# Kernel tuning notes

Hardware: AMD Instinct MI355X
Metric: run time of the kernel (lower is better)

Reference implementation:

```python
import jax, jax.numpy as jnp
import numpy as np

B, T, D, H = 64, 512, 512, 512

def setup_inputs() -> dict:
    key = jax.random.key(0)
    ks = jax.random.split(key, 9)
    std = 0.01
    return {
        "X": jax.random.normal(ks[0], (B, T, D), jnp.float32),
        "W_xi": std * jax.random.normal(ks[1], (D, H), jnp.float32),
        "W_hi": std * jax.random.normal(ks[2], (H, H), jnp.float32),
        "b_i": jnp.zeros((H,), jnp.float32),
        "W_xf": std * jax.random.normal(ks[3], (D, H), jnp.float32),
        "W_hf": std * jax.random.normal(ks[4], (H, H), jnp.float32),
        "b_f": jnp.zeros((H,), jnp.float32),
        "W_xo": std * jax.random.normal(ks[5], (D, H), jnp.float32),
        "W_ho": std * jax.random.normal(ks[6], (H, H), jnp.float32),
        "b_o": jnp.zeros((H,), jnp.float32),
        "W_xc": std * jax.random.normal(ks[7], (D, H), jnp.float32),
        "W_hc": std * jax.random.normal(ks[8], (H, H), jnp.float32),
        "b_c": jnp.zeros((H,), jnp.float32),
    }


def _lstm(X, W_xi, W_hi, b_i, W_xf, W_hf, b_f, W_xo, W_ho, b_o, W_xc, W_hc, b_c):
    # Fuse the 4 gate weight matrices into single GEMMs (same math as 8
    # separate matmuls in the original).
    W_x = jnp.concatenate([W_xi, W_xf, W_xo, W_xc], axis=1)  # [D, 4H]
    W_h = jnp.concatenate([W_hi, W_hf, W_ho, W_hc], axis=1)  # [H, 4H]
    b = jnp.concatenate([b_i, b_f, b_o, b_c], axis=0)        # [4H]
    H_dim = W_hi.shape[0]
    Bsz = X.shape[0]
    # Precompute input projections for all steps: [T, B, 4H]
    Xg = jnp.einsum('btd,dg->tbg', X, W_x) + b

    def step(carry, xg):
        h, c = carry
        g = xg + h @ W_h                              # [B, 4H]
        I = jax.nn.sigmoid(g[:, :H_dim])
        F = jax.nn.sigmoid(g[:, H_dim:2 * H_dim])
        O = jax.nn.sigmoid(g[:, 2 * H_dim:3 * H_dim])
        Cd = jnp.tanh(g[:, 3 * H_dim:])
        c = F * c + I * Cd
        h = O * jnp.tanh(c)
        return (h, c), h

    h0 = jnp.zeros((Bsz, H_dim), X.dtype)
    c0 = jnp.zeros((Bsz, H_dim), X.dtype)
    _, hs = jax.lax.scan(step, (h0, c0), Xg)          # hs: [T, B, H]
    return jnp.transpose(hs, (1, 0, 2))               # [B, T, H] (return_sequences=True)


def reference(X, W_xi, W_hi, b_i, W_xf, W_hf, b_f, W_xo, W_ho, b_o, W_xc, W_hc, b_c):
    return _lstm(X, W_xi, W_hi, b_i, W_xf, W_hf, b_f, W_xo, W_ho, b_o, W_xc, W_hc, b_c)
```

## Files before the change

kernel.cpp:

```cpp
#include <hip/hip_runtime.h>

#define TT 512
#define BSZ 64
#define DD 512
#define HH 512
#define NGROUP 4
#define GBLK 64
#define GBATCH 16
#define NT 512

#define PART_SP 40
#define PART_BB 1284

struct Params {
    const float* X;
    const float* Wx[4];
    const float* Wh[4];
    const float* bias[4];
    float* Y;
    float* hbuf;
    unsigned int* ctr;
};

__device__ __forceinline__ float fast_sigmoid(float x) {
    return 1.0f / (1.0f + __expf(-x));
}

__device__ __forceinline__ float fast_tanh(float x) {
    float ax = fabsf(x);
    float e  = __expf(-2.0f * ax);
    float r  = (1.0f - e) / (1.0f + e);
    return copysignf(r, x);
}

__device__ __forceinline__ float dpp_xor8_add(float v) {
    int pv = __builtin_amdgcn_update_dpp(0, __float_as_int(v),
                                         0x128 , 0xf, 0xf, true);
    return v + __int_as_float(pv);
}

__global__ void init_ws(float* hbuf, unsigned int* ctr) {
    int i = blockIdx.x * blockDim.x + threadIdx.x;
    int stride = gridDim.x * blockDim.x;
    for (int k = i; k < 2 * BSZ * HH; k += stride)
        __hip_atomic_store(&hbuf[k], 0.0f, __ATOMIC_RELAXED, __HIP_MEMORY_SCOPE_AGENT);
    if (i < 8 * 64)
        __hip_atomic_store(&ctr[i], 0u, __ATOMIC_RELAXED, __HIP_MEMORY_SCOPE_AGENT);
}

__global__ __launch_bounds__(NT, 1) void lstm_persist(Params p) {
    __shared__ float xs[GBATCH * DD];
    __shared__ float hs[GBATCH * HH];
    __shared__ float part[16 * PART_BB];

    const int bid  = blockIdx.x;
    const int g    = (bid & 7) >> 1;
    const int k    = ((bid >> 3) << 1) | (bid & 1);
    const int tid  = threadIdx.x;
    const int u    = tid & 7;
    const int s    = tid >> 3;
    const int kb   = s * 8;
    const int jc   = k * 8 + u;
    const int b0   = g * GBATCH;

    float4 wx4[4][2], wh4[4][2];
#pragma unroll
    for (int g4 = 0; g4 < 4; ++g4) {
        const float* WxG = p.Wx[g4];
        const float* WhG = p.Wh[g4];
#pragma unroll
        for (int k4 = 0; k4 < 2; ++k4) {
            int kk = kb + k4 * 4;
            wx4[g4][k4] = make_float4(WxG[(kk + 0) * HH + jc], WxG[(kk + 1) * HH + jc],
                                      WxG[(kk + 2) * HH + jc], WxG[(kk + 3) * HH + jc]);
            wh4[g4][k4] = make_float4(WhG[(kk + 0) * HH + jc], WhG[(kk + 1) * HH + jc],
                                      WhG[(kk + 2) * HH + jc], WhG[(kk + 3) * HH + jc]);
        }
    }

    const int bbu = tid >> 3;
    const int jju = tid & 7;
    const int ju  = k * 8 + jju;
    float cst = 0.0f;
    float bI = 0.f, bF = 0.f, bO = 0.f, bC = 0.f;
    if (tid < 128) {
        bI = p.bias[0][ju];
        bF = p.bias[1][ju];
        bO = p.bias[2][ju];
        bC = p.bias[3][ju];
    }

    unsigned int* ctrp = p.ctr + g * 64;
    const float4* xsrc = (const float4*)p.X;
    float4* xs4 = (float4*)xs;
    float4* hs4 = (float4*)hs;

#define ACC4(A, V, W) \
    A = fmaf((V).x, (W).x, A); A = fmaf((V).y, (W).y, A); \
    A = fmaf((V).z, (W).z, A); A = fmaf((V).w, (W).w, A);

    for (int t = 0; t < TT; ++t) {
#pragma unroll
        for (int uu = 0; uu < 4; ++uu) {
            int idx = tid + uu * NT;
            int b   = idx >> 7;
            int dd  = idx & 127;
            xs4[b * 128 + dd] = xsrc[((size_t)(b0 + b) * TT + t) * 128 + dd];
        }
        __syncthreads();

        float acc[4][16];
#pragma unroll
        for (int g4 = 0; g4 < 4; ++g4)
#pragma unroll
            for (int bb = 0; bb < 16; ++bb) acc[g4][bb] = 0.0f;
#pragma unroll
        for (int k4 = 0; k4 < 2; ++k4) {
#pragma unroll
            for (int bb = 0; bb < 16; ++bb) {
                float4 xv = xs4[bb * 128 + s * 2 + k4];
                ACC4(acc[0][bb], xv, wx4[0][k4]);
                ACC4(acc[1][bb], xv, wx4[1][k4]);
                ACC4(acc[2][bb], xv, wx4[2][k4]);
                ACC4(acc[3][bb], xv, wx4[3][k4]);
                if ((bb & 3) == 3) __builtin_amdgcn_sched_barrier(0);
            }
        }

        if (tid == 0) {
            const unsigned int need = (unsigned int)(GBLK * t);
            while (__hip_atomic_load(ctrp, __ATOMIC_RELAXED, __HIP_MEMORY_SCOPE_AGENT) < need) {
                __builtin_amdgcn_s_sleep(2);
            }
        }
        __syncthreads();

        {
            const unsigned long long* hsrc =
                (const unsigned long long*)(p.hbuf + (size_t)(t & 1) * BSZ * HH);
            unsigned long long tmpu[8];
#pragma unroll
            for (int uu = 0; uu < 8; ++uu) {
                int idx = tid + uu * NT;
                int b   = idx >> 8;
                int d   = idx & 255;
                tmpu[uu] = __hip_atomic_load(&hsrc[(size_t)(b0 + b) * 256 + d],
                                             __ATOMIC_RELAXED, __HIP_MEMORY_SCOPE_AGENT);
            }
            unsigned long long* hsu = (unsigned long long*)hs;
#pragma unroll
            for (int uu = 0; uu < 8; ++uu)
                hsu[tid + uu * NT] = tmpu[uu];
        }
        __syncthreads();

#pragma unroll
        for (int k4 = 0; k4 < 2; ++k4) {
#pragma unroll
            for (int bb = 0; bb < 16; ++bb) {
                float4 hv = hs4[bb * 128 + s * 2 + k4];
                ACC4(acc[0][bb], hv, wh4[0][k4]);
                ACC4(acc[1][bb], hv, wh4[1][k4]);
                ACC4(acc[2][bb], hv, wh4[2][k4]);
                ACC4(acc[3][bb], hv, wh4[3][k4]);
                if ((bb & 3) == 3) __builtin_amdgcn_sched_barrier(0);
            }
        }

#pragma unroll
        for (int g4 = 0; g4 < 4; ++g4)
#pragma unroll
            for (int bb = 0; bb < 16; ++bb)
                acc[g4][bb] = dpp_xor8_add(acc[g4][bb]);
        {
            const int sp = s >> 1;
            float* dst = &part[sp * PART_SP + (s & 1) * 16 + u];
            if ((s & 1) == 0) {
#pragma unroll
                for (int bb = 0; bb < 16; ++bb) {
                    dst[bb * PART_BB + 0] = acc[0][bb];
                    dst[bb * PART_BB + 8] = acc[1][bb];
                }
            } else {
#pragma unroll
                for (int bb = 0; bb < 16; ++bb) {
                    dst[bb * PART_BB + 0] = acc[2][bb];
                    dst[bb * PART_BB + 8] = acc[3][bb];
                }
            }
        }
        __syncthreads();

        if (tid < 128) {
            float v0 = bI, v1 = bF, v2 = bO, v3 = bC;
            const float* pr = &part[bbu * PART_BB + jju];
#pragma unroll
            for (int ss = 0; ss < 32; ++ss) {
                v0 += pr[ss * PART_SP + 0];
                v1 += pr[ss * PART_SP + 8];
                v2 += pr[ss * PART_SP + 16];
                v3 += pr[ss * PART_SP + 24];
            }
            float I  = fast_sigmoid(v0);
            float F  = fast_sigmoid(v1);
            float O  = fast_sigmoid(v2);
            float Cd = fast_tanh(v3);
            cst = fmaf(F, cst, I * Cd);
            float h = O * fast_tanh(cst);
            __hip_atomic_store(&p.hbuf[(size_t)((t + 1) & 1) * BSZ * HH + (b0 + bbu) * HH + ju],
                               h, __ATOMIC_RELAXED, __HIP_MEMORY_SCOPE_AGENT);
            p.Y[((size_t)(b0 + bbu) * TT + t) * HH + ju] = h;
        }
        __syncthreads();

        if (tid == 0) {
            __hip_atomic_fetch_add(ctrp, 1u, __ATOMIC_RELAXED, __HIP_MEMORY_SCOPE_AGENT);
        }
    }
#undef ACC4
}

extern "C" void kernel_launch(void* const* d_in, const int* in_sizes, int n_in,
                              void* d_out, int out_size, void* d_ws, size_t ws_size,
                              hipStream_t stream) {
    Params p;
    p.X       = (const float*)d_in[0];
    p.Wx[0]   = (const float*)d_in[1];
    p.Wh[0]   = (const float*)d_in[2];
    p.bias[0] = (const float*)d_in[3];
    p.Wx[1]   = (const float*)d_in[4];
    p.Wh[1]   = (const float*)d_in[5];
    p.bias[1] = (const float*)d_in[6];
    p.Wx[2]   = (const float*)d_in[7];
    p.Wh[2]   = (const float*)d_in[8];
    p.bias[2] = (const float*)d_in[9];
    p.Wx[3]   = (const float*)d_in[10];
    p.Wh[3]   = (const float*)d_in[11];
    p.bias[3] = (const float*)d_in[12];
    p.Y       = (float*)d_out;
    p.hbuf    = (float*)d_ws;
    p.ctr     = (unsigned int*)((char*)d_ws + (size_t)2 * BSZ * HH * sizeof(float));

    init_ws<<<64, 256, 0, stream>>>(p.hbuf, p.ctr);

    lstm_persist<<<dim3(256), dim3(NT), 0, stream>>>(p);
}
```

Measured before the change: 3.506 ms.

## Prefetch next-step X into registers and overlap h load with x-projection half

Moves the per-step X tile load out of the critical path: the next timestep's X slice is prefetched into registers while the h buffer load is in flight, then written to shared memory after the partial-sum stores, removing one barrier per step. The x-projection is split into two halves so the second half runs after the h loads are issued, hiding global-load latency behind FMAs. It adds register pressure (hreg, xreg) on top of the already large accumulator set, which could cause spills or lower occupancy.

After: 4.475 ms. 27.6% more time.

```diff
diff --git a/kernel.cpp b/kernel.cpp
--- a/kernel.cpp
+++ b/kernel.cpp
@@ -94,37 +94,35 @@
     const float4* xsrc = (const float4*)p.X;
     float4* xs4 = (float4*)xs;
     float4* hs4 = (float4*)hs;
+    unsigned long long* hsu = (unsigned long long*)hs;
 
 #define ACC4(A, V, W) \
     A = fmaf((V).x, (W).x, A); A = fmaf((V).y, (W).y, A); \
     A = fmaf((V).z, (W).z, A); A = fmaf((V).w, (W).w, A);
 
+#pragma unroll
+    for (int uu = 0; uu < 4; ++uu) {
+        int idx = tid + uu * NT;
+        int b   = idx >> 7;
+        int dd  = idx & 127;
+        xs4[b * 128 + dd] = xsrc[((size_t)(b0 + b) * TT + 0) * 128 + dd];
+    }
+    __syncthreads();
+
     for (int t = 0; t < TT; ++t) {
-#pragma unroll
-        for (int uu = 0; uu < 4; ++uu) {
-            int idx = tid + uu * NT;
-            int b   = idx >> 7;
-            int dd  = idx & 127;
-            xs4[b * 128 + dd] = xsrc[((size_t)(b0 + b) * TT + t) * 128 + dd];
-        }
-        __syncthreads();
-
         float acc[4][16];
 #pragma unroll
         for (int g4 = 0; g4 < 4; ++g4)
 #pragma unroll
             for (int bb = 0; bb < 16; ++bb) acc[g4][bb] = 0.0f;
 #pragma unroll
-        for (int k4 = 0; k4 < 2; ++k4) {
-#pragma unroll
-            for (int bb = 0; bb < 16; ++bb) {
-                float4 xv = xs4[bb * 128 + s * 2 + k4];
-                ACC4(acc[0][bb], xv, wx4[0][k4]);
-                ACC4(acc[1][bb], xv, wx4[1][k4]);
-                ACC4(acc[2][bb], xv, wx4[2][k4]);
-                ACC4(acc[3][bb], xv, wx4[3][k4]);
-                if ((bb & 3) == 3) __builtin_amdgcn_sched_barrier(0);
-            }
+        for (int bb = 0; bb < 16; ++bb) {
+            float4 xv = xs4[bb * 128 + s * 2 + 0];
+            ACC4(acc[0][bb], xv, wx4[0][0]);
+            ACC4(acc[1][bb], xv, wx4[1][0]);
+            ACC4(acc[2][bb], xv, wx4[2][0]);
+            ACC4(acc[3][bb], xv, wx4[3][0]);
+            if ((bb & 3) == 3) __builtin_amdgcn_sched_barrier(0);
         }
 
         if (tid == 0) {
@@ -135,23 +133,44 @@
         }
         __syncthreads();
 
+        unsigned long long hreg[8];
         {
             const unsigned long long* hsrc =
                 (const unsigned long long*)(p.hbuf + (size_t)(t & 1) * BSZ * HH);
-            unsigned long long tmpu[8];
 #pragma unroll
             for (int uu = 0; uu < 8; ++uu) {
                 int idx = tid + uu * NT;
                 int b   = idx >> 8;
                 int d   = idx & 255;
-                tmpu[uu] = __hip_atomic_load(&hsrc[(size_t)(b0 + b) * 256 + d],
+                hreg[uu] = __hip_atomic_load(&hsrc[(size_t)(b0 + b) * 256 + d],
                                              __ATOMIC_RELAXED, __HIP_MEMORY_SCOPE_AGENT);
             }
-            unsigned long long* hsu = (unsigned long long*)hs;
-#pragma unroll
-            for (int uu = 0; uu < 8; ++uu)
-                hsu[tid + uu * NT] = tmpu[uu];
-        }
+        }
+        float4 xreg[4];
+        if (t + 1 < TT) {
+#pragma unroll
+            for (int uu = 0; uu < 4; ++uu) {
+                int idx = tid + uu * NT;
+                int b   = idx >> 7;
+                int dd  = idx & 127;
+                xreg[uu] = xsrc[((size_t)(b0 + b) * TT + (t + 1)) * 128 + dd];
+            }
+        }
+        __builtin_amdgcn_sched_barrier(0);
+
+#pragma unroll
+        for (int bb = 0; bb < 16; ++bb) {
+            float4 xv = xs4[bb * 128 + s * 2 + 1];
+            ACC4(acc[0][bb], xv, wx4[0][1]);
+            ACC4(acc[1][bb], xv, wx4[1][1]);
+            ACC4(acc[2][bb], xv, wx4[2][1]);
+            ACC4(acc[3][bb], xv, wx4[3][1]);
+            if ((bb & 3) == 3) __builtin_amdgcn_sched_barrier(0);
+        }
+
+#pragma unroll
+        for (int uu = 0; uu < 8; ++uu)
+            hsu[tid + uu * NT] = hreg[uu];
         __syncthreads();
 
 #pragma unroll
@@ -187,6 +206,16 @@
                     dst[bb * PART_BB + 0] = acc[2][bb];
                     dst[bb * PART_BB + 8] = acc[3][bb];
                 }
+            }
+        }
+
+        if (t + 1 < TT) {
+#pragma unroll
+            for (int uu = 0; uu < 4; ++uu) {
+                int idx = tid + uu * NT;
+                int b   = idx >> 7;
+                int dd  = idx & 127;
+                xs4[b * 128 + dd] = xreg[uu];
             }
         }
         __syncthreads();
```
